# Kernel tuning notes

Measured on AMD Instinct MI355X. Metric: run time of the kernel, lower is better.

Reference implementation:

```python
import jax, jax.numpy as jnp
import numpy as np

N_GROUPS = 8
TOPK_GROUPS = 4
TOPK = 8
ROUTE_SCALE = 2.5


def setup_inputs() -> dict:
    key = jax.random.key(0)
    k1, k2, k3 = jax.random.split(key, 3)
    T, D, E = 8192, 7168, 256
    x = jax.random.normal(k1, (T, D), dtype=jnp.float32)
    weight = jax.random.normal(k2, (E, D), dtype=jnp.float32) * 0.02
    bias = jax.random.normal(k3, (E,), dtype=jnp.float32) * 0.02
    return {"x": x, "weight": weight, "bias": bias}


def reference(x, weight, bias):
    T = x.shape[0]
    # gate linear + sigmoid scores (score_func == 'sigmoid', computed in fp32)
    logits = jnp.einsum("td,ed->te", x, weight)  # [T, E]
    scores = jax.nn.sigmoid(logits.astype(jnp.float32))
    origin_scores = scores
    s = scores + bias  # bias present since dim == 7168
    # grouped scores: [T, G, E/G]
    sg = s.reshape(T, N_GROUPS, -1)
    # bias branch: group score = sum of top-2 per group
    top2, _ = jax.lax.top_k(sg, 2)
    group_scores = top2.sum(axis=-1)  # [T, G]
    # keep top `topk_groups` groups, zero out the rest
    _, gidx = jax.lax.top_k(group_scores, TOPK_GROUPS)  # [T, topk_groups]
    mask = jax.nn.one_hot(gidx, N_GROUPS, dtype=sg.dtype).sum(axis=1)  # [T, G]
    s_masked = (sg * mask[:, :, None]).reshape(T, -1)  # [T, E]
    # per-token expert top-k on masked scores
    _, expert_indices = jax.lax.top_k(s_masked, TOPK)  # [T, topk]
    # gather unbiased scores, normalize (sigmoid branch), scale
    weights = jnp.take_along_axis(origin_scores, expert_indices, axis=-1)
    weights = weights / weights.sum(axis=-1, keepdims=True)
    weights = weights * ROUTE_SCALE
    return weights.astype(x.dtype), expert_indices
```

## Files before the change

### kernel.cpp

```cpp
#include <hip/hip_runtime.h>
#include <cmath>

#define TT 8192
#define NE 256
#define ND 7168
#define NGRP 8
#define TOPKG 4
#define TOPK 8
#define ROUTE_SCALE 2.5f

#define NKT (ND / 32)
#define NNT (NE / 16)

#define TM 128
#define XPITCH 40
#define BSTRN ((size_t)NKT * 512)

typedef _Float16 half8_ __attribute__((ext_vector_type(8)));
typedef _Float16 half4_ __attribute__((ext_vector_type(4)));
typedef float float4_ __attribute__((ext_vector_type(4)));

#define BAR() asm volatile("s_waitcnt lgkmcnt(0)\n\ts_barrier" ::: "memory")

__global__ __launch_bounds__(256) void conv_w_kernel(
    const float* __restrict__ w, _Float16* __restrict__ whF,
    _Float16* __restrict__ wlF)
{
    const int gid  = blockIdx.x * 256 + threadIdx.x;
    const int lane = gid & 63;
    const int pair = gid >> 6;
    const int kt   = pair % NKT;
    const int nt   = pair / NKT;
    const int n  = nt * 16 + (lane & 15);
    const int kb = kt * 32 + (lane >> 4) * 8;
    const float* src = w + (size_t)n * ND + kb;
    const float4 v0 = *reinterpret_cast<const float4*>(src);
    const float4 v1 = *reinterpret_cast<const float4*>(src + 4);
    const float vs[8] = {v0.x, v0.y, v0.z, v0.w, v1.x, v1.y, v1.z, v1.w};
    half8_ h, l;
    #pragma unroll
    for (int j = 0; j < 8; ++j) {
        const _Float16 hi = (_Float16)vs[j];
        h[j] = hi;
        l[j] = (_Float16)(vs[j] - (float)hi);
    }
    const size_t off = ((size_t)pair * 64 + lane) * 8;
    *reinterpret_cast<half8_*>(whF + off) = h;
    *reinterpret_cast<half8_*>(wlF + off) = l;
}

__global__ __launch_bounds__(512, 2) void gemm_kernel(
    const float* __restrict__ x, const _Float16* __restrict__ whF,
    const _Float16* __restrict__ wlF, float* __restrict__ partial,
    int K_slice, int gsh)
{
    __shared__ _Float16 XhL[2][TM * XPITCH];
    __shared__ _Float16 XlL[2][TM * XPITCH];

    const int tid  = threadIdx.x;
    const int lane = tid & 63;
    const int wid  = tid >> 6;
    const int nq   = wid & 3;
    const int th   = wid >> 2;

    const int L    = blockIdx.x;
    const int xcd  = L & 7;
    const int slot = L >> 3;
    const int ks   = xcd >> gsh;
    const int bx   = (slot << gsh) | (xcd & ((1 << gsh) - 1));

    const int t0   = bx * TM;
    const int kbeg = ks * K_slice;
    const int kt0  = kbeg >> 5;
    const int nchunks = K_slice >> 5;

    const int q  = lane >> 4;
    const int cn = lane & 15;
    const int srow0 = tid >> 3;
    const int sc4   = tid & 7;

    float4_ acc[4][4];
    #pragma unroll
    for (int i = 0; i < 4; ++i)
        #pragma unroll
        for (int j = 0; j < 4; ++j) acc[i][j] = (float4_)0.0f;

    const float* xp0 = x + (size_t)(t0 + srow0) * ND + kbeg + sc4 * 4;
    const float* xp1 = xp0 + (size_t)64 * ND;
    const _Float16* bh0 = whF + (size_t)(nq * 4) * BSTRN + (size_t)kt0 * 512 + lane * 8;
    const _Float16* bl0 = wlF + (size_t)(nq * 4) * BSTRN + (size_t)kt0 * 512 + lane * 8;

    float4 xv[2][2];
    half8_ Bf[2][8];

    xv[0][0] = *reinterpret_cast<const float4*>(xp0);
    xv[0][1] = *reinterpret_cast<const float4*>(xp1);
    xv[1][0] = *reinterpret_cast<const float4*>(xp0 + 32);
    xv[1][1] = *reinterpret_cast<const float4*>(xp1 + 32);
    #pragma unroll
    for (int ntl = 0; ntl < 4; ++ntl) {
        Bf[0][ntl * 2 + 0] = *reinterpret_cast<const half8_*>(bh0 + (size_t)ntl * BSTRN);
        Bf[0][ntl * 2 + 1] = *reinterpret_cast<const half8_*>(bl0 + (size_t)ntl * BSTRN);
    }
    #pragma unroll
    for (int i = 0; i < 2; ++i) {
        const float4 v = xv[0][i];
        const float vs[4] = {v.x, v.y, v.z, v.w};
        half4_ h, l;
        #pragma unroll
        for (int j = 0; j < 4; ++j) {
            const _Float16 hi = (_Float16)vs[j];
            h[j] = hi; l[j] = (_Float16)(vs[j] - (float)hi);
        }
        const int soff = (srow0 + i * 64) * XPITCH + sc4 * 4;
        *reinterpret_cast<half4_*>(&XhL[0][soff]) = h;
        *reinterpret_cast<half4_*>(&XlL[0][soff]) = l;
    }
    BAR();

#define STEP(P, C)                                                           \
    {                                                                        \
        if ((C) + 2 < nchunks) {  \
            xv[P][0] = *reinterpret_cast<const float4*>(xp0 + ((C) + 2) * 32); \
            xv[P][1] = *reinterpret_cast<const float4*>(xp1 + ((C) + 2) * 32); \
        }                                                                    \
        if ((C) + 1 < nchunks) {                     \
            _Pragma("unroll")                                                \
            for (int ntl = 0; ntl < 4; ++ntl) {                              \
                Bf[(P) ^ 1][ntl * 2 + 0] = *reinterpret_cast<const half8_*>( \
                    bh0 + (size_t)ntl * BSTRN + ((C) + 1) * 512);            \
                Bf[(P) ^ 1][ntl * 2 + 1] = *reinterpret_cast<const half8_*>( \
                    bl0 + (size_t)ntl * BSTRN + ((C) + 1) * 512);            \
            }                                                                \
        }                                                                    \
        half8_ ah[4], al[4];                                                 \
        _Pragma("unroll")                                                    \
        for (int mt = 0; mt < 4; ++mt) {                                     \
            ah[mt] = *reinterpret_cast<const half8_*>(                       \
                &XhL[P][(th * 64 + mt * 16 + cn) * XPITCH + q * 8]);         \
            al[mt] = *reinterpret_cast<const half8_*>(                       \
                &XlL[P][(th * 64 + mt * 16 + cn) * XPITCH + q * 8]);         \
        }                                                                    \
        __builtin_amdgcn_s_setprio(1);                                       \
        _Pragma("unroll")                                                    \
        for (int mt = 0; mt < 4; ++mt)                                       \
            _Pragma("unroll")                                                \
            for (int ntl = 0; ntl < 4; ++ntl) {                              \
                acc[mt][ntl] = __builtin_amdgcn_mfma_f32_16x16x32_f16(       \
                    ah[mt], Bf[P][ntl * 2 + 0], acc[mt][ntl], 0, 0, 0);      \
                acc[mt][ntl] = __builtin_amdgcn_mfma_f32_16x16x32_f16(       \
                    al[mt], Bf[P][ntl * 2 + 0], acc[mt][ntl], 0, 0, 0);      \
                acc[mt][ntl] = __builtin_amdgcn_mfma_f32_16x16x32_f16(       \
                    ah[mt], Bf[P][ntl * 2 + 1], acc[mt][ntl], 0, 0, 0);      \
            }                                                                \
        __builtin_amdgcn_s_setprio(0);                                       \
        if ((C) + 1 < nchunks) {  \
            _Pragma("unroll")                                                \
            for (int i = 0; i < 2; ++i) {                                    \
                const float4 v = xv[(P) ^ 1][i];                             \
                const float vs[4] = {v.x, v.y, v.z, v.w};                    \
                half4_ h, l;                                                 \
                _Pragma("unroll")                                            \
                for (int j = 0; j < 4; ++j) {                                \
                    const _Float16 hi = (_Float16)vs[j];                     \
                    h[j] = hi; l[j] = (_Float16)(vs[j] - (float)hi);         \
                }                                                            \
                const int soff = (srow0 + i * 64) * XPITCH + sc4 * 4;        \
                *reinterpret_cast<half4_*>(&XhL[(P) ^ 1][soff]) = h;         \
                *reinterpret_cast<half4_*>(&XlL[(P) ^ 1][soff]) = l;         \
            }                                                                \
        }                                                                    \
        BAR();                                                               \
    }

    for (int c = 0; c < nchunks; c += 2) {
        STEP(0, c)
        STEP(1, c + 1)
    }
#undef STEP

    #pragma unroll
    for (int mt = 0; mt < 4; ++mt)
        #pragma unroll
        for (int r = 0; r < 4; ++r) {
            const int t = t0 + th * 64 + mt * 16 + q * 4 + r;
            float* rowp = partial + ((size_t)ks * TT + t) * NE;
            #pragma unroll
            for (int ntl = 0; ntl < 4; ++ntl)
                rowp[nq * 64 + ntl * 16 + cn] = acc[mt][ntl][r];
        }
}

__global__ __launch_bounds__(256) void routing_kernel(
    const float* __restrict__ partial, const float* __restrict__ bias,
    float* __restrict__ out_w, float* __restrict__ out_i, int kslices)
{
    const int lane = threadIdx.x & 63;
    const int t = blockIdx.x * 4 + (threadIdx.x >> 6);

    float4 a = make_float4(0.f, 0.f, 0.f, 0.f);
    for (int s = 0; s < kslices; ++s) {
        const float4 p = *reinterpret_cast<const float4*>(
            partial + ((size_t)s * TT + t) * NE + lane * 4);
        a.x += p.x; a.y += p.y; a.z += p.z; a.w += p.w;
    }
    const float4 b4 = *reinterpret_cast<const float4*>(bias + lane * 4);
    const float lg[4] = {a.x, a.y, a.z, a.w};
    const float bs[4] = {b4.x, b4.y, b4.z, b4.w};
    float sg[4], sv[4];
    #pragma unroll
    for (int j = 0; j < 4; ++j) {
        sg[j] = 1.0f / (1.0f + expf(-lg[j]));
        sv[j] = sg[j] + bs[j];
    }

    float m1 = -1e30f, m2 = -1e30f;
    #pragma unroll
    for (int j = 0; j < 4; ++j) {
        if (sv[j] > m1)      { m2 = m1; m1 = sv[j]; }
        else if (sv[j] > m2) { m2 = sv[j]; }
    }
    #pragma unroll
    for (int off = 1; off <= 4; off <<= 1) {
        const float o1 = __shfl_xor(m1, off, 64);
        const float o2 = __shfl_xor(m2, off, 64);
        if (o1 > m1) { m2 = fmaxf(m1, o2); m1 = o1; }
        else         { m2 = fmaxf(m2, o1); }
    }
    const float gs = m1 + m2;

    float gv[NGRP];
    #pragma unroll
    for (int g = 0; g < NGRP; ++g) gv[g] = __shfl(gs, g * 8, 64);
    unsigned keep = 0;
    #pragma unroll
    for (int r = 0; r < TOPKG; ++r) {
        int best = 0; float bvv = -1e30f;
        #pragma unroll
        for (int g = 0; g < NGRP; ++g) {
            const bool taken = (keep >> g) & 1u;
            if (!taken && gv[g] > bvv) { bvv = gv[g]; best = g; }
        }
        keep |= 1u << best;
    }

    const bool kept = (keep >> (lane >> 3)) & 1u;
    float rv[4];
    #pragma unroll
    for (int j = 0; j < 4; ++j) rv[j] = kept ? sv[j] : 0.0f;

    float wsum = 0.f, myw = 0.f;
    int myi = 0;
    #pragma unroll
    for (int r = 0; r < TOPK; ++r) {
        float bv = -1e30f, bo = 0.f; int bi = 0x7fffffff;
        #pragma unroll
        for (int j = 0; j < 4; ++j)
            if (rv[j] > bv) { bv = rv[j]; bi = lane * 4 + j; bo = sg[j]; }
        #pragma unroll
        for (int off = 1; off < 64; off <<= 1) {
            const float ov = __shfl_xor(bv, off, 64);
            const int   oi = __shfl_xor(bi, off, 64);
            const float oo = __shfl_xor(bo, off, 64);
            if (ov > bv || (ov == bv && oi < bi)) { bv = ov; bi = oi; bo = oo; }
        }
        if ((bi >> 2) == lane) rv[bi & 3] = -1e30f;
        wsum += bo;
        if (lane == r) { myw = bo; myi = bi; }
    }
    const float scale = ROUTE_SCALE / wsum;
    if (lane < TOPK) {
        out_w[(size_t)t * TOPK + lane] = myw * scale;
        out_i[(size_t)t * TOPK + lane] = (float)myi;
    }
}

extern "C" void kernel_launch(void* const* d_in, const int* in_sizes, int n_in,
                              void* d_out, int out_size, void* d_ws, size_t ws_size,
                              hipStream_t stream) {
    const float* x    = (const float*)d_in[0];
    const float* w    = (const float*)d_in[1];
    const float* bias = (const float*)d_in[2];

    float* out_w = (float*)d_out;
    float* out_i = (float*)d_out + (size_t)TT * TOPK;

    const size_t wfrag_bytes = (size_t)NE * ND * sizeof(_Float16);
    _Float16* whF = (_Float16*)d_ws;
    _Float16* wlF = (_Float16*)((char*)d_ws + wfrag_bytes);
    float* partial = (float*)((char*)d_ws + 2 * wfrag_bytes);

    const size_t part1 = (size_t)TT * NE * sizeof(float);
    int kslices = 1, gsh = 3;
    if      (ws_size >= 2 * wfrag_bytes + 4 * part1) { kslices = 4; gsh = 1; }
    else if (ws_size >= 2 * wfrag_bytes + 2 * part1) { kslices = 2; gsh = 2; }
    const int K_slice = ND / kslices;

    conv_w_kernel<<<(NNT * NKT * 64) / 256, 256, 0, stream>>>(w, whF, wlF);

    gemm_kernel<<<(TT / TM) * kslices, 512, 0, stream>>>(x, whF, wlF, partial,
                                                         K_slice, gsh);

    routing_kernel<<<TT / 4, 256, 0, stream>>>(partial, bias, out_w, out_i, kslices);
}
```

Measured before the change: 380.2 us.

## Switch GEMM from 16x16x32 to 32x32x16 MFMA tiles with matching weight layout

Replaces the 16x16x32 f16 MFMA tiling with 32x32x16 MFMA instructions. Each wave now holds a 2x2 grid of 32x32 accumulators instead of 4x4 16x16 ones. The weight fragment layout written by the conversion kernel, the shared-memory A-fragment reads and the output store mapping all change to match. The larger MFMA shape issues fewer instructions per unit of work and reuses operands better, but it alters LDS access patterns and register usage.

```diff
diff --git a/kernel.cpp b/kernel.cpp
--- a/kernel.cpp
+++ b/kernel.cpp
@@ -9,16 +9,16 @@
 #define TOPK 8
 #define ROUTE_SCALE 2.5f
 
-#define NKT (ND / 32)
-#define NNT (NE / 16)
+#define NT32 (NE / 32)
+#define NK16 (ND / 16)
 
 #define TM 128
 #define XPITCH 40
-#define BSTRN ((size_t)NKT * 512)
+#define BSTRN2 ((size_t)NK16 * 512)
 
 typedef _Float16 half8_ __attribute__((ext_vector_type(8)));
 typedef _Float16 half4_ __attribute__((ext_vector_type(4)));
-typedef float float4_ __attribute__((ext_vector_type(4)));
+typedef float float16_ __attribute__((ext_vector_type(16)));
 
 #define BAR() asm volatile("s_waitcnt lgkmcnt(0)\n\ts_barrier" ::: "memory")
 
@@ -29,10 +29,10 @@
     const int gid  = blockIdx.x * 256 + threadIdx.x;
     const int lane = gid & 63;
     const int pair = gid >> 6;
-    const int kt   = pair % NKT;
-    const int nt   = pair / NKT;
-    const int n  = nt * 16 + (lane & 15);
-    const int kb = kt * 32 + (lane >> 4) * 8;
+    const int kk   = pair % NK16;
+    const int nt   = pair / NK16;
+    const int n  = nt * 32 + (lane & 31);
+    const int kb = kk * 16 + (lane >> 5) * 8;
     const float* src = w + (size_t)n * ND + kb;
     const float4 v0 = *reinterpret_cast<const float4*>(src);
     const float4 v1 = *reinterpret_cast<const float4*>(src + 4);
@@ -71,24 +71,24 @@
 
     const int t0   = bx * TM;
     const int kbeg = ks * K_slice;
-    const int kt0  = kbeg >> 5;
+    const int kk0  = kbeg >> 4;
     const int nchunks = K_slice >> 5;
 
-    const int q  = lane >> 4;
-    const int cn = lane & 15;
+    const int q5 = lane >> 5;
+    const int cn = lane & 31;
     const int srow0 = tid >> 3;
     const int sc4   = tid & 7;
 
-    float4_ acc[4][4];
-    #pragma unroll
-    for (int i = 0; i < 4; ++i)
-        #pragma unroll
-        for (int j = 0; j < 4; ++j) acc[i][j] = (float4_)0.0f;
+    float16_ acc[2][2];
+    #pragma unroll
+    for (int i = 0; i < 2; ++i)
+        #pragma unroll
+        for (int j = 0; j < 2; ++j) acc[i][j] = (float16_)0.0f;
 
     const float* xp0 = x + (size_t)(t0 + srow0) * ND + kbeg + sc4 * 4;
     const float* xp1 = xp0 + (size_t)64 * ND;
-    const _Float16* bh0 = whF + (size_t)(nq * 4) * BSTRN + (size_t)kt0 * 512 + lane * 8;
-    const _Float16* bl0 = wlF + (size_t)(nq * 4) * BSTRN + (size_t)kt0 * 512 + lane * 8;
+    const _Float16* bh0 = whF + (size_t)(nq * 2) * BSTRN2 + (size_t)kk0 * 512 + lane * 8;
+    const _Float16* bl0 = wlF + (size_t)(nq * 2) * BSTRN2 + (size_t)kk0 * 512 + lane * 8;
 
     float4 xv[2][2];
     half8_ Bf[2][8];
@@ -98,10 +98,14 @@
     xv[1][0] = *reinterpret_cast<const float4*>(xp0 + 32);
     xv[1][1] = *reinterpret_cast<const float4*>(xp1 + 32);
     #pragma unroll
-    for (int ntl = 0; ntl < 4; ++ntl) {
-        Bf[0][ntl * 2 + 0] = *reinterpret_cast<const half8_*>(bh0 + (size_t)ntl * BSTRN);
-        Bf[0][ntl * 2 + 1] = *reinterpret_cast<const half8_*>(bl0 + (size_t)ntl * BSTRN);
-    }
+    for (int nt2 = 0; nt2 < 2; ++nt2)
+        #pragma unroll
+        for (int s = 0; s < 2; ++s) {
+            Bf[0][nt2 * 4 + s * 2 + 0] = *reinterpret_cast<const half8_*>(
+                bh0 + (size_t)nt2 * BSTRN2 + s * 512);
+            Bf[0][nt2 * 4 + s * 2 + 1] = *reinterpret_cast<const half8_*>(
+                bl0 + (size_t)nt2 * BSTRN2 + s * 512);
+        }
     #pragma unroll
     for (int i = 0; i < 2; ++i) {
         const float4 v = xv[0][i];
@@ -126,33 +130,46 @@
         }                                                                    \
         if ((C) + 1 < nchunks) {                     \
             _Pragma("unroll")                                                \
-            for (int ntl = 0; ntl < 4; ++ntl) {                              \
-                Bf[(P) ^ 1][ntl * 2 + 0] = *reinterpret_cast<const half8_*>( \
-                    bh0 + (size_t)ntl * BSTRN + ((C) + 1) * 512);            \
-                Bf[(P) ^ 1][ntl * 2 + 1] = *reinterpret_cast<const half8_*>( \
-                    bl0 + (size_t)ntl * BSTRN + ((C) + 1) * 512);            \
+            for (int nt2 = 0; nt2 < 2; ++nt2)                                \
+                _Pragma("unroll")                                            \
+                for (int s = 0; s < 2; ++s) {                                \
+                    Bf[(P) ^ 1][nt2 * 4 + s * 2 + 0] =                       \
+                        *reinterpret_cast<const half8_*>(                    \
+                            bh0 + (size_t)nt2 * BSTRN2 +                     \
+                            (2 * ((C) + 1) + s) * 512);                      \
+                    Bf[(P) ^ 1][nt2 * 4 + s * 2 + 1] =                       \
+                        *reinterpret_cast<const half8_*>(                    \
+                            bl0 + (size_t)nt2 * BSTRN2 +                     \
+                            (2 * ((C) + 1) + s) * 512);                      \
+                }                                                            \
+        }                                                                    \
+        half8_ ah[2][2], al[2][2];                     \
+        _Pragma("unroll")                                                    \
+        for (int rt = 0; rt < 2; ++rt)                                       \
+            _Pragma("unroll")                                                \
+            for (int s = 0; s < 2; ++s) {                                    \
+                const int ro = (th * 64 + rt * 32 + cn) * XPITCH             \
+                               + s * 16 + q5 * 8;                            \
+                ah[rt][s] = *reinterpret_cast<const half8_*>(&XhL[P][ro]);   \
+                al[rt][s] = *reinterpret_cast<const half8_*>(&XlL[P][ro]);   \
             }                                                                \
-        }                                                                    \
-        half8_ ah[4], al[4];                                                 \
-        _Pragma("unroll")                                                    \
-        for (int mt = 0; mt < 4; ++mt) {                                     \
-            ah[mt] = *reinterpret_cast<const half8_*>(                       \
-                &XhL[P][(th * 64 + mt * 16 + cn) * XPITCH + q * 8]);         \
-            al[mt] = *reinterpret_cast<const half8_*>(                       \
-                &XlL[P][(th * 64 + mt * 16 + cn) * XPITCH + q * 8]);         \
-        }                                                                    \
         __builtin_amdgcn_s_setprio(1);                                       \
         _Pragma("unroll")                                                    \
-        for (int mt = 0; mt < 4; ++mt)                                       \
+        for (int rt = 0; rt < 2; ++rt)                                       \
             _Pragma("unroll")                                                \
-            for (int ntl = 0; ntl < 4; ++ntl) {                              \
-                acc[mt][ntl] = __builtin_amdgcn_mfma_f32_16x16x32_f16(       \
-                    ah[mt], Bf[P][ntl * 2 + 0], acc[mt][ntl], 0, 0, 0);      \
-                acc[mt][ntl] = __builtin_amdgcn_mfma_f32_16x16x32_f16(       \
-                    al[mt], Bf[P][ntl * 2 + 0], acc[mt][ntl], 0, 0, 0);      \
-                acc[mt][ntl] = __builtin_amdgcn_mfma_f32_16x16x32_f16(       \
-                    ah[mt], Bf[P][ntl * 2 + 1], acc[mt][ntl], 0, 0, 0);      \
-            }                                                                \
+            for (int nt2 = 0; nt2 < 2; ++nt2)                                \
+                _Pragma("unroll")                                            \
+                for (int s = 0; s < 2; ++s) {                                \
+                    acc[rt][nt2] = __builtin_amdgcn_mfma_f32_32x32x16_f16(   \
+                        ah[rt][s], Bf[P][nt2 * 4 + s * 2 + 0],               \
+                        acc[rt][nt2], 0, 0, 0);                              \
+                    acc[rt][nt2] = __builtin_amdgcn_mfma_f32_32x32x16_f16(   \
+                        al[rt][s], Bf[P][nt2 * 4 + s * 2 + 0],               \
+                        acc[rt][nt2], 0, 0, 0);                              \
+                    acc[rt][nt2] = __builtin_amdgcn_mfma_f32_32x32x16_f16(   \
+                        ah[rt][s], Bf[P][nt2 * 4 + s * 2 + 1],               \
+                        acc[rt][nt2], 0, 0, 0);                              \
+                }                                                            \
         __builtin_amdgcn_s_setprio(0);                                       \
         if ((C) + 1 < nchunks) {  \
             _Pragma("unroll")                                                \
@@ -180,15 +197,16 @@
 #undef STEP
 
     #pragma unroll
-    for (int mt = 0; mt < 4; ++mt)
-        #pragma unroll
-        for (int r = 0; r < 4; ++r) {
-            const int t = t0 + th * 64 + mt * 16 + q * 4 + r;
-            float* rowp = partial + ((size_t)ks * TT + t) * NE;
+    for (int rt = 0; rt < 2; ++rt)
+        #pragma unroll
+        for (int nt2 = 0; nt2 < 2; ++nt2)
             #pragma unroll
-            for (int ntl = 0; ntl < 4; ++ntl)
-                rowp[nq * 64 + ntl * 16 + cn] = acc[mt][ntl][r];
-        }
+            for (int reg = 0; reg < 16; ++reg) {
+                const int t = t0 + th * 64 + rt * 32 +
+                              (reg & 3) + 8 * (reg >> 2) + 4 * q5;
+                partial[((size_t)ks * TT + t) * NE + nq * 64 + nt2 * 32 + cn] =
+                    acc[rt][nt2][reg];
+            }
 }
 
 __global__ __launch_bounds__(256) void routing_kernel(
@@ -296,7 +314,7 @@
     else if (ws_size >= 2 * wfrag_bytes + 2 * part1) { kslices = 2; gsh = 2; }
     const int K_slice = ND / kslices;
 
-    conv_w_kernel<<<(NNT * NKT * 64) / 256, 256, 0, stream>>>(w, whF, wlF);
+    conv_w_kernel<<<(NT32 * NK16 * 64) / 256, 256, 0, stream>>>(w, whF, wlF);
 
     gemm_kernel<<<(TT / TM) * kslices, 512, 0, stream>>>(x, whF, wlF, partial,
                                                          K_slice, gsh);
```

After: 378.6 us. Within noise of the previous version (-0.4%).
